# Performance work log

Measured on AMD Instinct MI355X. Metric: run time of the kernel, lower is better.

Reference implementation:

```python
import jax, jax.numpy as jnp
import numpy as np
import math

B_GRAPHS = 256
L_NODES = 64
N_NODES = B_GRAPHS * L_NODES
N_EDGES = N_NODES * 4
HEADS = 8
D_INNER = 512
N_DAGS = 1
DIAMETER = 64


def setup_inputs() -> dict:
    key = jax.random.key(0)
    ks = jax.random.split(key, 8)
    x = jax.random.normal(ks[0], (N_NODES, D_INNER), jnp.float32)
    B = jax.random.normal(ks[1], (N_NODES, D_INNER), jnp.float32)
    C = jax.random.normal(ks[2], (N_NODES, D_INNER), jnp.float32)
    dt = jax.random.normal(ks[3], (N_NODES, N_DAGS * HEADS * 2), jnp.float32)
    dt_edge = jax.random.normal(ks[4], (N_EDGES, N_DAGS * HEADS), jnp.float32)
    # DAG edges: within each graph, src_local < dst_local (gap 1..7) -> strictly upper triangular
    u = jax.random.randint(ks[5], (N_EDGES,), 0, L_NODES - 1)
    gap = jax.random.randint(ks[6], (N_EDGES,), 1, 8)
    v = jnp.minimum(u + gap, L_NODES - 1)
    graph = jnp.arange(N_EDGES) // (N_EDGES // B_GRAPHS)
    edge_index = jnp.stack([graph * L_NODES + u, graph * L_NODES + v]).astype(jnp.int32)
    data_batch = (jnp.arange(N_NODES) // L_NODES).astype(jnp.int32)
    dag_masks = jnp.ones((N_DAGS, N_EDGES), jnp.float32)
    # dt_bias init as in module __init__ (inverse softplus of dt in [1e-3, 1e-1])
    rng = np.random.default_rng(0)
    dtv = np.exp(rng.uniform(size=(HEADS,)) * (math.log(0.1) - math.log(0.001)) + math.log(0.001))
    dtv = np.clip(dtv, 1e-4, None)
    dt_bias = jnp.asarray(dtv + np.log(-np.expm1(-dtv)), jnp.float32)
    D = jnp.ones((HEADS,), jnp.float32)
    return dict(x=x, B=B, C=C, dt=dt, dt_edge=dt_edge, dt_bias=dt_bias, D=D,
                dag_masks=dag_masks, edge_index=edge_index, data_batch=data_batch,
                diameter=DIAMETER)


def _repeated_squaring_inverse(A, diam):
    # (I - A)^{-1} = prod_k (I + A^{2^k}) for nilpotent A; O(log diam) matmuls
    j = 2 ** int(math.ceil(math.log2(diam)))
    I = jnp.eye(A.shape[-1], dtype=A.dtype)
    last = A
    M = I + A
    for _ in range(2, int(math.log2(j)) + 1):
        last = last @ last
        M = M @ (I + last)
    return M


def reference(x, B, C, dt, dt_edge, dt_bias, D, dag_masks, edge_index, data_batch, diameter):
    N, din = x.shape
    g, E = dag_masks.shape
    n = dt_bias.shape[0]
    b = int(data_batch[-1]) + 1
    l = N // b  # equal-size graphs -> dense batching is a reshape, mask all-True
    h = din // n
    src, dst = edge_index[0], edge_index[1]

    # dt_node: (N, g*n*c) -> (c, g, n, N); softplus(dt + bias)
    c = dt.shape[1] // (g * n)
    dtn = dt.reshape(N, g, n, c).transpose(3, 1, 2, 0)
    dtn = jax.nn.softplus(dtn + dt_bias[None, None, :, None])
    dte = dt_edge.reshape(E, g, n).transpose(1, 2, 0)  # (g,n,E)
    dte = jax.nn.softplus(dte + dt_bias[None, :, None])

    dt_s, dt_t = dtn[0], dtn[1]
    dt_sum = (dt_s[:, :, src] + dt_t[:, :, dst] + dte) / np.sqrt(3.0)  # (g,n,E)
    dt_exp = jnp.exp(-dt_sum)
    msk = dag_masks[:, None, :]
    dt_sum = dt_sum * msk
    dt_exp = dt_exp * msk

    # dense adjacency with per-edge attrs; note 'b l1 l2 (g n) -> b g n l2 l1' transpose
    b_e = src // l
    sl = src % l
    dl = dst % l
    attr = dt_exp.transpose(2, 0, 1).reshape(E, g * n)
    adj = jnp.zeros((b, l, l, g * n), x.dtype).at[b_e, sl, dl].add(attr)
    A = adj.reshape(b, l, l, g, n).transpose(0, 3, 4, 2, 1)  # (b,g,n,l,l)

    # normalize_mat: sqrt outer product of in-degree counts, clamped at 1
    ec = jnp.zeros((g, N), x.dtype).at[:, dst].add(dag_masks)
    ec_dense = ec.T.reshape(b, l, g)
    outer = jnp.sqrt(jnp.einsum('blg,btg->bglt', ec_dense, ec_dense))
    outer = jnp.where(outer < 1.0, 1.0, outer)
    A = A / outer[:, :, None]

    dnorm = jnp.zeros((g, n, N), x.dtype).at[:, :, dst].add(dt_sum)
    dnorm = dnorm.transpose(2, 0, 1).reshape(b, l, g, n).transpose(0, 2, 3, 1)  # (b,g,n,l)

    A2 = A.reshape(b, g * n, l, l).astype(jnp.float32)
    L = _repeated_squaring_inverse(A2, int(diameter))
    L = L.reshape(b, g, n, l, l) * dnorm[..., None]

    x4 = x.reshape(b, l, n, h).transpose(0, 2, 1, 3)  # (b,n,l,h)
    B3 = B.reshape(b, l, -1)
    C3 = C.reshape(b, l, -1)
    # y = einsum(C,L,B,x) with B/C broadcast over (g,n): fold C.B^T into L
    CB = jnp.einsum('bld,btd->blt', C3, B3)
    M = L * CB[:, None, None]
    y = jnp.einsum('bgnlt,bnth->bgnlh', M, x4)
    y = y + x4[:, None] * D[None, None, :, None, None]
    y = y.transpose(0, 3, 1, 2, 4).reshape(N, g, n * h)  # b g n l h -> (N, g, n*h)
    y = y.sum(axis=1) / np.sqrt(g)
    return y
```

## Files before the change

### kernel.cpp

```cpp
#include <hip/hip_runtime.h>
#include <math.h>

#define NGRAPH 256
#define LNODE  64
#define HEADS  8
#define DIN    512
#define EPG    256
#define NEDGE  65536

typedef short bf16x8 __attribute__((ext_vector_type(8)));
typedef float f32x4 __attribute__((ext_vector_type(4)));

__device__ __forceinline__ float softplusf(float v) {
    return (v > 20.f) ? v : log1pf(expf(v));
}
__device__ __forceinline__ unsigned short f2bf(float f) {
    union { float f; unsigned u; } c; c.f = f;
    unsigned r = c.u + 0x7fffu + ((c.u >> 16) & 1u);
    return (unsigned short)(r >> 16);
}
__device__ __forceinline__ float bf2f(unsigned short h) {
    union { float f; unsigned u; } c; c.u = ((unsigned)h) << 16;
    return c.f;
}

__global__ __launch_bounds__(256) void cb_kernel(const float* __restrict__ Bm,
                                                 const float* __restrict__ Cm,
                                                 float* __restrict__ CBp,
                                                 int dper, int tposed) {
    int b = blockIdx.x;
    int slice = blockIdx.y;
    __shared__ float Cs[64 * 68];
    __shared__ float Bs[64 * 68];
    int tid = threadIdx.x;
    int ti = tid >> 4, tj = tid & 15;
    float acc[4][4] = {};
    const float* Cg = Cm + (size_t)b * 64 * DIN;
    const float* Bg = Bm + (size_t)b * 64 * DIN;
    int d_lo = slice * dper;
    for (int d0 = d_lo; d0 < d_lo + dper; d0 += 64) {
        __syncthreads();
        #pragma unroll
        for (int k = 0; k < 4; ++k) {
            int f = k * 256 + tid;
            int row = f >> 4;
            int c4 = (f & 15) << 2;
            *(float4*)(Cs + row * 68 + c4) = *(const float4*)(Cg + row * DIN + d0 + c4);
            *(float4*)(Bs + row * 68 + c4) = *(const float4*)(Bg + row * DIN + d0 + c4);
        }
        __syncthreads();
        for (int d = 0; d < 64; d += 4) {
            float4 cr[4], br[4];
            #pragma unroll
            for (int r = 0; r < 4; ++r) cr[r] = *(const float4*)(Cs + (4 * ti + r) * 68 + d);
            #pragma unroll
            for (int c = 0; c < 4; ++c) br[c] = *(const float4*)(Bs + (4 * tj + c) * 68 + d);
            #pragma unroll
            for (int r = 0; r < 4; ++r)
                #pragma unroll
                for (int c = 0; c < 4; ++c)
                    acc[r][c] += cr[r].x * br[c].x + cr[r].y * br[c].y +
                                 cr[r].z * br[c].z + cr[r].w * br[c].w;
        }
    }
    float* outp = CBp + ((size_t)slice * NGRAPH + b) * 4096;
    if (!tposed) {
        #pragma unroll
        for (int r = 0; r < 4; ++r)
            *(float4*)(outp + (4 * ti + r) * 64 + 4 * tj) =
                make_float4(acc[r][0], acc[r][1], acc[r][2], acc[r][3]);
    } else {
        #pragma unroll
        for (int r = 0; r < 4; ++r)
            #pragma unroll
            for (int c = 0; c < 4; ++c)
                outp[(4 * tj + c) * 64 + (4 * ti + r)] = acc[r][c];
    }
}

__global__ __launch_bounds__(256, 4) void fused2_kernel(const float* __restrict__ x,
                                                        const float* __restrict__ dt,
                                                        const float* __restrict__ dt_edge,
                                                        const float* __restrict__ dt_bias,
                                                        const float* __restrict__ Dp,
                                                        const float* __restrict__ dag_masks,
                                                        const int* __restrict__ edge_index,
                                                        const float* __restrict__ CBp,
                                                        float* __restrict__ out,
                                                        int nslice) {
    int b = blockIdx.x;
    int head = blockIdx.y;
    __shared__ unsigned short CBsh[64 * 64];
    __shared__ unsigned short Wl[64 * 72];
    __shared__ unsigned short Xt[64 * 72];
    __shared__ float Ab[512];
    __shared__ float dnsh[64];
    __shared__ float ecsh[64];
    __shared__ float dts[64];
    __shared__ float dtt[64];
    int tid = threadIdx.x;
    int w = tid >> 6;
    int lane = tid & 63;

    for (int s4 = tid; s4 < 1024; s4 += 256) {
        float4 v = make_float4(0.f, 0.f, 0.f, 0.f);
        for (int s = 0; s < nslice; ++s) {
            float4 p = *(const float4*)(CBp + ((size_t)s * NGRAPH + b) * 4096 + s4 * 4);
            v.x += p.x; v.y += p.y; v.z += p.z; v.w += p.w;
        }
        unsigned short* q = &CBsh[s4 * 4];
        q[0] = f2bf(v.x); q[1] = f2bf(v.y); q[2] = f2bf(v.z); q[3] = f2bf(v.w);
    }
    const float* xg0 = x + (size_t)b * 64 * DIN + head * 64;
    #pragma unroll
    for (int k = 0; k < 4; ++k) {
        int s = k * 256 + tid;
        int t = s >> 4;
        int e0 = (s & 15) << 2;
        float4 v = *(const float4*)(xg0 + (size_t)t * DIN + e0);
        Xt[(e0 + 0) * 72 + t] = f2bf(v.x);
        Xt[(e0 + 1) * 72 + t] = f2bf(v.y);
        Xt[(e0 + 2) * 72 + t] = f2bf(v.z);
        Xt[(e0 + 3) * 72 + t] = f2bf(v.w);
    }
    for (int k = tid; k < 512; k += 256) Ab[k] = 0.f;
    float bias = dt_bias[head];
    if (tid < 64) {
        dnsh[tid] = 0.f;
        ecsh[tid] = 0.f;
        int node = b * 64 + tid;
        dts[tid] = softplusf(dt[node * 16 + head * 2 + 0] + bias);
        dtt[tid] = softplusf(dt[node * 16 + head * 2 + 1] + bias);
    }
    __syncthreads();

    {
        int e = b * EPG + tid;
        int sl = edge_index[e] & 63;
        int dl = edge_index[NEDGE + e] & 63;
        float mk = dag_masks[e];
        float de = softplusf(dt_edge[e * HEADS + head] + bias);
        float dsum = (dts[sl] + dtt[dl] + de) * 0.57735026918962576451f;
        float dexp = expf(-dsum);
        atomicAdd(&Ab[dl * 8 + (dl - sl)], dexp * mk);
        atomicAdd(&dnsh[dl], dsum * mk);
        atomicAdd(&ecsh[dl], mk);
    }
    __syncthreads();

    for (int k = tid; k < 512; k += 256) {
        int i = k >> 3, d = k & 7;
        int src = i - d;
        if (d >= 1 && src >= 0) {
            float den = sqrtf(ecsh[i] * ecsh[src]);
            if (den < 1.f) den = 1.f;
            Ab[k] = Ab[k] / den;
        }
    }
    __syncthreads();

    if (w == 0) {
        int j = lane;
        float Dh = Dp[head];
        float mwin[7] = {0.f, 0.f, 0.f, 0.f, 0.f, 0.f, 0.f};
        for (int i = 0; i < 64; ++i) {
            float mi = (j == i) ? 1.f : 0.f;
            #pragma unroll
            for (int s = 0; s < 7; ++s) mi += Ab[i * 8 + s + 1] * mwin[s];
            float wv = mi * bf2f(CBsh[i * 64 + j]) * dnsh[i];
            if (j == i) wv += Dh;
            Wl[i * 72 + j] = f2bf(wv);
            #pragma unroll
            for (int s = 6; s > 0; --s) mwin[s] = mwin[s - 1];
            mwin[0] = mi;
        }
    }
    __syncthreads();

    {
        int m = lane & 15;
        int quad = lane >> 4;
        bf16x8 a0 = *(const bf16x8*)(&Wl[(16 * w + m) * 72 + quad * 8]);
        bf16x8 a1 = *(const bf16x8*)(&Wl[(16 * w + m) * 72 + 32 + quad * 8]);
        float* og = out + ((size_t)b * 64) * DIN + head * 64;
        #pragma unroll
        for (int eb = 0; eb < 4; ++eb) {
            bf16x8 b0 = *(const bf16x8*)(&Xt[(eb * 16 + m) * 72 + quad * 8]);
            bf16x8 b1 = *(const bf16x8*)(&Xt[(eb * 16 + m) * 72 + 32 + quad * 8]);
            f32x4 acc = {0.f, 0.f, 0.f, 0.f};
            acc = __builtin_amdgcn_mfma_f32_16x16x32_bf16(a0, b0, acc, 0, 0, 0);
            acc = __builtin_amdgcn_mfma_f32_16x16x32_bf16(a1, b1, acc, 0, 0, 0);
            #pragma unroll
            for (int r = 0; r < 4; ++r) {
                int row = 16 * w + quad * 4 + r;
                og[(size_t)row * DIN + eb * 16 + m] = acc[r];
            }
        }
    }
}

__global__ __launch_bounds__(256, 4) void fused_kernel(const float* __restrict__ x,
                                                       const float* __restrict__ dt,
                                                       const float* __restrict__ dt_edge,
                                                       const float* __restrict__ dt_bias,
                                                       const float* __restrict__ Dp,
                                                       const float* __restrict__ dag_masks,
                                                       const int* __restrict__ edge_index,
                                                       const float* __restrict__ CBt,
                                                       float* __restrict__ out,
                                                       int nslice) {
    int b = blockIdx.x;
    int head = blockIdx.y;
    __shared__ float Ab[64 * 8];
    __shared__ float Mt[64 * 68];
    __shared__ float Xs[64 * 64];
    __shared__ float dnsh[64];
    __shared__ float ecsh[64];
    __shared__ float dts[64];
    __shared__ float dtt[64];
    int tid = threadIdx.x;

    int t4 = tid >> 2;
    int ib = (tid & 3) << 4;
    float4 cbsum[4];
    #pragma unroll
    for (int g = 0; g < 4; ++g) cbsum[g] = make_float4(0.f, 0.f, 0.f, 0.f);
    for (int s = 0; s < nslice; ++s) {
        const float* p = CBt + ((size_t)s * NGRAPH + b) * 4096 + t4 * 64 + ib;
        #pragma unroll
        for (int g = 0; g < 4; ++g) {
            float4 v = *(const float4*)(p + 4 * g);
            cbsum[g].x += v.x; cbsum[g].y += v.y; cbsum[g].z += v.z; cbsum[g].w += v.w;
        }
    }
    const float* xg0 = x + ((size_t)b * 64) * DIN + head * 64;
    #pragma unroll
    for (int k = 0; k < 4; ++k) {
        int s = k * 256 + tid;
        int row = s >> 4;
        int c4 = (s & 15) << 2;
        *(float4*)(Xs + row * 64 + c4) = *(const float4*)(xg0 + (size_t)row * DIN + c4);
    }
    for (int k = tid; k < 512; k += 256) Ab[k] = 0.f;
    float bias = dt_bias[head];
    if (tid < 64) {
        dnsh[tid] = 0.f;
        ecsh[tid] = 0.f;
        int node = b * 64 + tid;
        dts[tid] = softplusf(dt[node * 16 + head * 2 + 0] + bias);
        dtt[tid] = softplusf(dt[node * 16 + head * 2 + 1] + bias);
    }
    __syncthreads();
    {
        int e = b * EPG + tid;
        int sl = edge_index[e] & 63;
        int dl = edge_index[NEDGE + e] & 63;
        float mk = dag_masks[e];
        float de = softplusf(dt_edge[e * HEADS + head] + bias);
        float dsum = (dts[sl] + dtt[dl] + de) * 0.57735026918962576451f;
        float dexp = expf(-dsum);
        atomicAdd(&Ab[dl * 8 + (dl - sl)], dexp * mk);
        atomicAdd(&dnsh[dl], dsum * mk);
        atomicAdd(&ecsh[dl], mk);
    }
    __syncthreads();
    for (int k = tid; k < 512; k += 256) {
        int i = k >> 3, d = k & 7;
        int src = i - d;
        if (d >= 1 && src >= 0) {
            float den = sqrtf(ecsh[i] * ecsh[src]);
            if (den < 1.f) den = 1.f;
            Ab[k] = Ab[k] / den;
        }
    }
    __syncthreads();
    if (tid < 64) {
        int j = tid;
        float mwin[7] = {0.f, 0.f, 0.f, 0.f, 0.f, 0.f, 0.f};
        for (int i = 0; i < 64; ++i) {
            float mi = (j == i) ? 1.f : 0.f;
            #pragma unroll
            for (int s = 0; s < 7; ++s) mi += Ab[i * 8 + s + 1] * mwin[s];
            Mt[j * 65 + i] = mi;
            #pragma unroll
            for (int s = 6; s > 0; --s) mwin[s] = mwin[s - 1];
            mwin[0] = mi;
        }
    }
    __syncthreads();
    {
        float wv[16];
        #pragma unroll
        for (int g = 0; g < 4; ++g) {
            float4 dn4 = *(const float4*)(dnsh + ib + 4 * g);
            wv[4 * g + 0] = Mt[t4 * 65 + ib + 4 * g + 0] * cbsum[g].x * dn4.x;
            wv[4 * g + 1] = Mt[t4 * 65 + ib + 4 * g + 1] * cbsum[g].y * dn4.y;
            wv[4 * g + 2] = Mt[t4 * 65 + ib + 4 * g + 2] * cbsum[g].z * dn4.z;
            wv[4 * g + 3] = Mt[t4 * 65 + ib + 4 * g + 3] * cbsum[g].w * dn4.w;
        }
        __syncthreads();
        #pragma unroll
        for (int g = 0; g < 4; ++g)
            *(float4*)(Mt + t4 * 68 + ib + 4 * g) =
                make_float4(wv[4 * g + 0], wv[4 * g + 1], wv[4 * g + 2], wv[4 * g + 3]);
    }
    __syncthreads();
    int ti = tid >> 4, tj = tid & 15;
    float acc[4][4] = {};
    #pragma unroll 4
    for (int t = 0; t < 64; ++t) {
        float4 w4 = *(const float4*)(Mt + t * 68 + 4 * ti);
        float4 xv = *(const float4*)(Xs + t * 64 + 4 * tj);
        acc[0][0] += w4.x * xv.x; acc[0][1] += w4.x * xv.y; acc[0][2] += w4.x * xv.z; acc[0][3] += w4.x * xv.w;
        acc[1][0] += w4.y * xv.x; acc[1][1] += w4.y * xv.y; acc[1][2] += w4.y * xv.z; acc[1][3] += w4.y * xv.w;
        acc[2][0] += w4.z * xv.x; acc[2][1] += w4.z * xv.y; acc[2][2] += w4.z * xv.z; acc[2][3] += w4.z * xv.w;
        acc[3][0] += w4.w * xv.x; acc[3][1] += w4.w * xv.y; acc[3][2] += w4.w * xv.z; acc[3][3] += w4.w * xv.w;
    }
    float Dh = Dp[head];
    #pragma unroll
    for (int r = 0; r < 4; ++r) {
        int i = 4 * ti + r;
        float4 xres = *(const float4*)(Xs + i * 64 + 4 * tj);
        float4 v;
        v.x = acc[r][0] + xres.x * Dh;
        v.y = acc[r][1] + xres.y * Dh;
        v.z = acc[r][2] + xres.z * Dh;
        v.w = acc[r][3] + xres.w * Dh;
        *(float4*)(out + ((size_t)(b * 64 + i)) * DIN + head * 64 + 4 * tj) = v;
    }
}

extern "C" void kernel_launch(void* const* d_in, const int* in_sizes, int n_in,
                              void* d_out, int out_size, void* d_ws, size_t ws_size,
                              hipStream_t stream) {
    const float* x        = (const float*)d_in[0];
    const float* Bm       = (const float*)d_in[1];
    const float* Cm       = (const float*)d_in[2];
    const float* dt       = (const float*)d_in[3];
    const float* dt_edge  = (const float*)d_in[4];
    const float* dt_bias  = (const float*)d_in[5];
    const float* Dp       = (const float*)d_in[6];
    const float* dag_mask = (const float*)d_in[7];
    const int*   edge_idx = (const int*)d_in[8];
    float* out = (float*)d_out;

    const size_t CBSLICE = (size_t)NGRAPH * 4096 * 4;
    float* CBp = (float*)d_ws;

    if (ws_size >= 2 * CBSLICE) {
        int nslice = 2;
        cb_kernel<<<dim3(NGRAPH, nslice), 256, 0, stream>>>(Bm, Cm, CBp, DIN / nslice, 0);
        fused2_kernel<<<dim3(NGRAPH, HEADS), 256, 0, stream>>>(x, dt, dt_edge, dt_bias, Dp,
                                                               dag_mask, edge_idx, CBp, out, nslice);
    } else {
        int nslice = 1;
        cb_kernel<<<dim3(NGRAPH, nslice), 256, 0, stream>>>(Bm, Cm, CBp, DIN / nslice, 1);
        fused_kernel<<<dim3(NGRAPH, HEADS), 256, 0, stream>>>(x, dt, dt_edge, dt_bias, Dp,
                                                              dag_mask, edge_idx, CBp, out, nslice);
    }
}
```

Baseline: 192.7 us.

## Warp-specialize fused2 prologue and prefetch X fragments before serial recurrence

```diff
diff --git a/kernel.cpp b/kernel.cpp
--- a/kernel.cpp
+++ b/kernel.cpp
@@ -78,7 +78,7 @@
     }
 }
 
-__global__ __launch_bounds__(256, 4) void fused2_kernel(const float* __restrict__ x,
+__global__ __launch_bounds__(256, 5) void fused2_kernel(const float* __restrict__ x,
                                                         const float* __restrict__ dt,
                                                         const float* __restrict__ dt_edge,
                                                         const float* __restrict__ dt_bias,
@@ -92,7 +92,7 @@
     int head = blockIdx.y;
     __shared__ unsigned short CBsh[64 * 64];
     __shared__ unsigned short Wl[64 * 72];
-    __shared__ unsigned short Xt[64 * 72];
+    __shared__ unsigned short Xt[64 * 66];
     __shared__ float Ab[512];
     __shared__ float dnsh[64];
     __shared__ float ecsh[64];
@@ -101,36 +101,36 @@
     int tid = threadIdx.x;
     int w = tid >> 6;
     int lane = tid & 63;
-
-    for (int s4 = tid; s4 < 1024; s4 += 256) {
-        float4 v = make_float4(0.f, 0.f, 0.f, 0.f);
-        for (int s = 0; s < nslice; ++s) {
-            float4 p = *(const float4*)(CBp + ((size_t)s * NGRAPH + b) * 4096 + s4 * 4);
-            v.x += p.x; v.y += p.y; v.z += p.z; v.w += p.w;
-        }
-        unsigned short* q = &CBsh[s4 * 4];
-        q[0] = f2bf(v.x); q[1] = f2bf(v.y); q[2] = f2bf(v.z); q[3] = f2bf(v.w);
-    }
+    float bias = dt_bias[head];
     const float* xg0 = x + (size_t)b * 64 * DIN + head * 64;
-    #pragma unroll
-    for (int k = 0; k < 4; ++k) {
-        int s = k * 256 + tid;
-        int t = s >> 4;
-        int e0 = (s & 15) << 2;
-        float4 v = *(const float4*)(xg0 + (size_t)t * DIN + e0);
-        Xt[(e0 + 0) * 72 + t] = f2bf(v.x);
-        Xt[(e0 + 1) * 72 + t] = f2bf(v.y);
-        Xt[(e0 + 2) * 72 + t] = f2bf(v.z);
-        Xt[(e0 + 3) * 72 + t] = f2bf(v.w);
-    }
-    for (int k = tid; k < 512; k += 256) Ab[k] = 0.f;
-    float bias = dt_bias[head];
-    if (tid < 64) {
-        dnsh[tid] = 0.f;
-        ecsh[tid] = 0.f;
-        int node = b * 64 + tid;
-        dts[tid] = softplusf(dt[node * 16 + head * 2 + 0] + bias);
-        dtt[tid] = softplusf(dt[node * 16 + head * 2 + 1] + bias);
+
+    if (w == 0) {
+        for (int it = 0; it < 16; ++it) {
+            int s4 = it * 64 + lane;
+            float4 v = *(const float4*)(CBp + (size_t)b * 4096 + s4 * 4);
+            for (int s = 1; s < nslice; ++s) {
+                float4 p = *(const float4*)(CBp + ((size_t)s * NGRAPH + b) * 4096 + s4 * 4);
+                v.x += p.x; v.y += p.y; v.z += p.z; v.w += p.w;
+            }
+            unsigned short* q = &CBsh[s4 * 4];
+            q[0] = f2bf(v.x); q[1] = f2bf(v.y); q[2] = f2bf(v.z); q[3] = f2bf(v.w);
+        }
+    } else {
+        for (int t = w - 1; t < 64; t += 3) {
+            float v = xg0[(size_t)t * DIN + lane];
+            Xt[lane * 66 + t] = f2bf(v);
+        }
+        if (w == 1) {
+            int node = b * 64 + lane;
+            dts[lane] = softplusf(dt[node * 16 + head * 2 + 0] + bias);
+            dtt[lane] = softplusf(dt[node * 16 + head * 2 + 1] + bias);
+        } else if (w == 2) {
+            #pragma unroll
+            for (int k = 0; k < 8; ++k) Ab[k * 64 + lane] = 0.f;
+        } else {
+            dnsh[lane] = 0.f;
+            ecsh[lane] = 0.f;
+        }
     }
     __syncthreads();
 
@@ -159,6 +159,20 @@
     }
     __syncthreads();
 
+    int m = lane & 15;
+    int quad = lane >> 4;
+    union { bf16x8 v; unsigned u[4]; } bf[4][2];
+    #pragma unroll
+    for (int eb = 0; eb < 4; ++eb) {
+        int n66 = (eb * 16 + m) * 66;
+        #pragma unroll
+        for (int h = 0; h < 2; ++h) {
+            int base = n66 + h * 32 + quad * 8;
+            #pragma unroll
+            for (int c = 0; c < 4; ++c)
+                bf[eb][h].u[c] = *(const unsigned*)(&Xt[base + 2 * c]);
+        }
+    }
     if (w == 0) {
         int j = lane;
         float Dh = Dp[head];
@@ -178,18 +192,14 @@
     __syncthreads();
 
     {
-        int m = lane & 15;
-        int quad = lane >> 4;
         bf16x8 a0 = *(const bf16x8*)(&Wl[(16 * w + m) * 72 + quad * 8]);
         bf16x8 a1 = *(const bf16x8*)(&Wl[(16 * w + m) * 72 + 32 + quad * 8]);
         float* og = out + ((size_t)b * 64) * DIN + head * 64;
         #pragma unroll
         for (int eb = 0; eb < 4; ++eb) {
-            bf16x8 b0 = *(const bf16x8*)(&Xt[(eb * 16 + m) * 72 + quad * 8]);
-            bf16x8 b1 = *(const bf16x8*)(&Xt[(eb * 16 + m) * 72 + 32 + quad * 8]);
             f32x4 acc = {0.f, 0.f, 0.f, 0.f};
-            acc = __builtin_amdgcn_mfma_f32_16x16x32_bf16(a0, b0, acc, 0, 0, 0);
-            acc = __builtin_amdgcn_mfma_f32_16x16x32_bf16(a1, b1, acc, 0, 0, 0);
+            acc = __builtin_amdgcn_mfma_f32_16x16x32_bf16(a0, bf[eb][0].v, acc, 0, 0, 0);
+            acc = __builtin_amdgcn_mfma_f32_16x16x32_bf16(a1, bf[eb][1].v, acc, 0, 0, 0);
             #pragma unroll
             for (int r = 0; r < 4; ++r) {
                 int row = 16 * w + quad * 4 + r;
```

Result: slower. 198.7 us (+3.1%).
